# Kernel tuning notes

Hardware: AMD Instinct MI355X
Metric: run time of the kernel (lower is better)

Reference implementation:

```python
import jax, jax.numpy as jnp
import numpy as np

IN_DIM = 256
BOTTLENECK = 32
QK_DIM = IN_DIM // BOTTLENECK  # 8


def setup_inputs() -> dict:
    key = jax.random.key(0)
    ks = jax.random.split(key, 10)
    B, C, W, H = 4, IN_DIM, 64, 64
    s = 0.05
    return {
        "x": jax.random.normal(ks[0], (B, C, W, H), jnp.float32),
        "k": jax.random.normal(ks[1], (B, C, W, H), jnp.float32),
        "q": jax.random.normal(ks[2], (B, C, W, H), jnp.float32),
        "Wq": jax.random.normal(ks[3], (QK_DIM, C), jnp.float32) * s,
        "bq": jax.random.normal(ks[4], (QK_DIM,), jnp.float32) * s,
        "Wk": jax.random.normal(ks[5], (QK_DIM, C), jnp.float32) * s,
        "bk": jax.random.normal(ks[6], (QK_DIM,), jnp.float32) * s,
        "Wv": jax.random.normal(ks[7], (C, C), jnp.float32) * s,
        "bv": jax.random.normal(ks[8], (C,), jnp.float32) * s,
        "gamma": jnp.array([0.5], jnp.float32),
    }


def reference(x, k, q, Wq, bq, Wk, bk, Wv, bv, gamma):
    B, C, W, H = x.shape
    N = W * H
    # 1x1 convs == per-pixel linear maps over channels; flatten spatial to N
    xf = x.reshape(B, C, N)
    kf = k.reshape(B, C, N)
    qf = q.reshape(B, C, N)
    # proj_query: (B, N, d); proj_key: (B, d, N)
    pq = jnp.einsum('dc,bcn->bnd', Wq, qf) + bq[None, None, :]
    pk = jnp.einsum('dc,bcn->bdn', Wk, kf) + bk[None, :, None]
    energy = jnp.einsum('bnd,bdm->bnm', pq, pk)  # (B, N, N), un-scaled
    attention = jax.nn.softmax(energy, axis=-1)
    pv = jnp.einsum('ec,bcn->ben', Wv, xf) + bv[None, :, None]  # (B, C, N)
    # out = bmm(value, attention^T): out[b,c,n] = sum_m pv[b,c,m] * attn[b,n,m]
    out = jnp.einsum('bcm,bnm->bcn', pv, attention)
    out = out.reshape(B, C, W, H)
    out = gamma[0] * out + x
    return out, attention
```

## Files before the change

kernel.cpp:

```cpp
#include <hip/hip_runtime.h>

#define B_ 4
#define C_ 256
#define N_ 4096
#define D_ 8

typedef float f32x4 __attribute__((ext_vector_type(4)));
typedef __bf16 bf16x8 __attribute__((ext_vector_type(8)));

union U16 {
  bf16x8 v;
  unsigned short u[8];
  uint4 q;
};

__device__ inline unsigned short f2bf(float f) {
  unsigned int u = __float_as_uint(f);
  u = (u + 0x7FFFu + ((u >> 16) & 1u)) >> 16;
  return (unsigned short)u;
}

#define AS1 __attribute__((address_space(1)))
#define AS3 __attribute__((address_space(3)))
__device__ __forceinline__ void g2l16(const void* g, void* l) {
  __builtin_amdgcn_global_load_lds((AS1 const void*)g, (AS3 void*)l, 16, 0, 0);
}

__global__ void __launch_bounds__(256) k_pqk(
    const float* __restrict__ q, const float* __restrict__ k,
    const float* __restrict__ Wq, const float* __restrict__ bq,
    const float* __restrict__ Wk, const float* __restrict__ bk,
    float* __restrict__ pq_g, float* __restrict__ pk_g) {
  int b = blockIdx.y, n0 = blockIdx.x * 64;
  int t = threadIdx.x, nl = t & 63, sub = t >> 6;
  int n = n0 + nl;
  float aq[D_], ak[D_];
#pragma unroll
  for (int d = 0; d < D_; ++d) { aq[d] = 0.f; ak[d] = 0.f; }
  const float* qp = q + ((size_t)(b * C_ + sub * 64)) * N_ + n;
  const float* kp = k + ((size_t)(b * C_ + sub * 64)) * N_ + n;
  for (int cc = 0; cc < 64; ++cc) {
    int c = sub * 64 + cc;
    float qv = qp[(size_t)cc * N_];
    float kv = kp[(size_t)cc * N_];
#pragma unroll
    for (int d = 0; d < D_; ++d) {
      aq[d] = fmaf(Wq[d * C_ + c], qv, aq[d]);
      ak[d] = fmaf(Wk[d * C_ + c], kv, ak[d]);
    }
  }
  __shared__ float red[4][64][16];
#pragma unroll
  for (int d = 0; d < D_; ++d) { red[sub][nl][d] = aq[d]; red[sub][nl][8 + d] = ak[d]; }
  __syncthreads();
  if (t < 64) {
#pragma unroll
    for (int d = 0; d < D_; ++d) {
      float s = red[0][t][d] + red[1][t][d] + red[2][t][d] + red[3][t][d] + bq[d];
      pq_g[((size_t)b * N_ + n0 + t) * D_ + d] = s;
      float s2 = red[0][t][8 + d] + red[1][t][8 + d] + red[2][t][8 + d] + red[3][t][8 + d] + bk[d];
      pk_g[((size_t)b * D_ + d) * N_ + n0 + t] = s2;
    }
  }
}

__global__ void __launch_bounds__(256) k_pv(
    const float* __restrict__ x, const float* __restrict__ Wv,
    const float* __restrict__ bv, unsigned short* __restrict__ pv_g) {
  int b = blockIdx.y, n0 = blockIdx.x * 64;
  int t = threadIdx.x, lane = t & 63, w = t >> 6;
  __shared__ unsigned short xs[64][264];
  {
    int nl = t & 63, sub = t >> 6;
    for (int i = 0; i < 64; ++i) {
      int c = i * 4 + sub;
      float xv = x[((size_t)(b * C_ + c)) * N_ + n0 + nl];
      xs[nl][c] = f2bf(xv);
    }
  }
  __syncthreads();
  int e0 = w * 64;
  f32x4 acc[4][4];
#pragma unroll
  for (int mf = 0; mf < 4; ++mf)
#pragma unroll
    for (int nf = 0; nf < 4; ++nf) acc[mf][nf] = (f32x4)0.f;

  int rsel = lane & 15, koff = (lane >> 4) * 8;
  for (int kc = 0; kc < 8; ++kc) {
    int cbase = kc * 32 + koff;
    U16 afr[4];
#pragma unroll
    for (int mf = 0; mf < 4; ++mf) {
      const float* wp = Wv + (size_t)(e0 + mf * 16 + rsel) * C_ + cbase;
      float4 w0 = *(const float4*)wp;
      float4 w1 = *(const float4*)(wp + 4);
      afr[mf].u[0] = f2bf(w0.x); afr[mf].u[1] = f2bf(w0.y);
      afr[mf].u[2] = f2bf(w0.z); afr[mf].u[3] = f2bf(w0.w);
      afr[mf].u[4] = f2bf(w1.x); afr[mf].u[5] = f2bf(w1.y);
      afr[mf].u[6] = f2bf(w1.z); afr[mf].u[7] = f2bf(w1.w);
    }
    U16 bfr[4];
#pragma unroll
    for (int nf = 0; nf < 4; ++nf)
      bfr[nf].q = *(const uint4*)&xs[nf * 16 + rsel][cbase];
#pragma unroll
    for (int mf = 0; mf < 4; ++mf)
#pragma unroll
      for (int nf = 0; nf < 4; ++nf)
        acc[mf][nf] = __builtin_amdgcn_mfma_f32_16x16x32_bf16(afr[mf].v, bfr[nf].v, acc[mf][nf], 0, 0, 0);
  }
  int rowsub = (lane >> 4) * 4;
#pragma unroll
  for (int mf = 0; mf < 4; ++mf) {
#pragma unroll
    for (int nf = 0; nf < 4; ++nf) {
      int n = n0 + nf * 16 + rsel;
#pragma unroll
      for (int j = 0; j < 4; ++j) {
        int e = e0 + mf * 16 + rowsub + j;
        float v = acc[mf][nf][j] + bv[e];
        pv_g[((size_t)(b * C_ + e)) * N_ + n] = f2bf(v);
      }
    }
  }
}

__global__ void __launch_bounds__(256) k_rowsum(
    const float* __restrict__ pq_g, const float* __restrict__ pk_g,
    float* __restrict__ rinv_g) {
  int b = blockIdx.y, n0 = blockIdx.x * 32;
  int t = threadIdx.x, lane = t & 63, w = t >> 6;
  int r0 = n0 + w * 8;
  float pqr[8][D_];
#pragma unroll
  for (int r = 0; r < 8; ++r) {
    const float4* pp = (const float4*)(pq_g + ((size_t)b * N_ + r0 + r) * D_);
    float4 a = pp[0], c4 = pp[1];
    pqr[r][0] = a.x; pqr[r][1] = a.y; pqr[r][2] = a.z; pqr[r][3] = a.w;
    pqr[r][4] = c4.x; pqr[r][5] = c4.y; pqr[r][6] = c4.z; pqr[r][7] = c4.w;
  }
  float s[8];
#pragma unroll
  for (int r = 0; r < 8; ++r) s[r] = 0.f;
  const float* pkb = pk_g + (size_t)b * D_ * N_;
  for (int tt = 0; tt < 64; ++tt) {
    int m = tt * 64 + lane;
    float pkr[D_];
#pragma unroll
    for (int d = 0; d < D_; ++d) pkr[d] = pkb[(size_t)d * N_ + m];
#pragma unroll
    for (int r = 0; r < 8; ++r) {
      float e = pqr[r][0] * pkr[0];
#pragma unroll
      for (int d = 1; d < D_; ++d) e = fmaf(pqr[r][d], pkr[d], e);
      s[r] += __expf(e);
    }
  }
#pragma unroll
  for (int r = 0; r < 8; ++r) {
    float v = s[r];
    for (int off = 32; off; off >>= 1) v += __shfl_xor(v, off);
    s[r] = v;
  }
  if (lane == 0) {
#pragma unroll
    for (int r = 0; r < 8; ++r) rinv_g[(size_t)b * N_ + r0 + r] = 1.0f / s[r];
  }
}

__global__ void __launch_bounds__(512, 1) k_fused(
    const float* __restrict__ pq_g, const float* __restrict__ pk_g,
    const float* __restrict__ rinv_g, const unsigned short* __restrict__ pv_g,
    const float* __restrict__ x, const float* __restrict__ gamma,
    float* __restrict__ out_g, float* __restrict__ attn_g) {
  int bx = blockIdx.x;
  int b = bx & 3, grp = bx >> 2;
  int n0 = grp * 32;
  int t = threadIdx.x, lane = t & 63, w = t >> 6;
  int rsel = lane & 15, g = lane >> 4, koff = g * 8;
  int c0 = w * 32;
  int r0 = n0 + w * 4;

  __shared__ unsigned short pvs[2][256][64];
  __shared__ unsigned short asl[2][32][72];

  float pqr[4][D_], rinv[4];
#pragma unroll
  for (int rr = 0; rr < 4; ++rr) {
    const float4* pp = (const float4*)(pq_g + ((size_t)b * N_ + r0 + rr) * D_);
    float4 a = pp[0], c4 = pp[1];
    pqr[rr][0] = a.x; pqr[rr][1] = a.y; pqr[rr][2] = a.z; pqr[rr][3] = a.w;
    pqr[rr][4] = c4.x; pqr[rr][5] = c4.y; pqr[rr][6] = c4.z; pqr[rr][7] = c4.w;
    rinv[rr] = rinv_g[(size_t)b * N_ + r0 + rr];
  }

  const float* pkb = pk_g + (size_t)b * D_ * N_;
  const unsigned short* pvb = pv_g + (size_t)b * C_ * N_;
  float* attb = attn_g + ((size_t)b * N_ + r0) * N_;

  f32x4 acc[2][2];
#pragma unroll
  for (int mf = 0; mf < 2; ++mf)
#pragma unroll
    for (int cf = 0; cf < 2; ++cf) acc[mf][cf] = (f32x4)0.f;

#define STAGEPV(dstbuf, M0)                                                   \
  {                                                                           \
    _Pragma("unroll")                                                         \
    for (int i = 0; i < 4; ++i) {                                             \
      int c = c0 + i * 8 + (lane >> 3);                                       \
      int seg = lane & 7;                                                     \
      g2l16(pvb + (size_t)c * N_ + (M0) + ((seg ^ (c & 7)) << 3),             \
            &pvs[dstbuf][c0 + i * 8][0]);                                     \
    }                                                                         \
  }

  STAGEPV(0, 0)
  float pkr[D_];
#pragma unroll
  for (int d = 0; d < D_; ++d) pkr[d] = pkb[(size_t)d * N_ + lane];

  int cur = 0;
  for (int tt = 0; tt < 64; ++tt) {
    int m0 = tt * 64;
    bool more = (tt + 1 < 64);
    if (more) STAGEPV(cur ^ 1, m0 + 64)
    float pkn[D_];
    if (more) {
#pragma unroll
      for (int d = 0; d < D_; ++d) pkn[d] = pkb[(size_t)d * N_ + m0 + 64 + lane];
    }
#pragma unroll
    for (int rr = 0; rr < 4; ++rr) {
      float e = pqr[rr][0] * pkr[0];
#pragma unroll
      for (int d = 1; d < D_; ++d) e = fmaf(pqr[rr][d], pkr[d], e);
      float a = __expf(e) * rinv[rr];
      __builtin_nontemporal_store(a, attb + (size_t)rr * N_ + m0 + lane);
      asl[cur][w * 4 + rr][lane] = f2bf(a);
    }
    asm volatile("s_waitcnt lgkmcnt(0)" ::: "memory");
    __builtin_amdgcn_s_barrier();
    {
      U16 afr[2][2], bfr[2][2];
#pragma unroll
      for (int kf = 0; kf < 2; ++kf) {
#pragma unroll
        for (int mf = 0; mf < 2; ++mf)
          afr[kf][mf].q = *(const uint4*)&asl[cur][mf * 16 + rsel][kf * 32 + koff];
#pragma unroll
        for (int cf = 0; cf < 2; ++cf) {
          int c = c0 + cf * 16 + rsel;
          int sg = kf * 4 + g;
          bfr[kf][cf].q = *(const uint4*)&pvs[cur][c][(sg ^ (c & 7)) * 8];
        }
      }
#pragma unroll
      for (int kf = 0; kf < 2; ++kf)
#pragma unroll
        for (int mf = 0; mf < 2; ++mf)
#pragma unroll
          for (int cf = 0; cf < 2; ++cf)
            acc[mf][cf] = __builtin_amdgcn_mfma_f32_16x16x32_bf16(
                afr[kf][mf].v, bfr[kf][cf].v, acc[mf][cf], 0, 0, 0);
    }
#pragma unroll
    for (int d = 0; d < D_; ++d) pkr[d] = pkn[d];
    cur ^= 1;
  }
#undef STAGEPV
  float gm = gamma[0];
  int rowsub = g * 4;
#pragma unroll
  for (int mf = 0; mf < 2; ++mf) {
#pragma unroll
    for (int cf = 0; cf < 2; ++cf) {
      int c = c0 + cf * 16 + rsel;
      int nrow = n0 + mf * 16 + rowsub;
      const float4 xv = *(const float4*)(x + ((size_t)(b * C_ + c)) * N_ + nrow);
      float4 o;
      o.x = gm * acc[mf][cf][0] + xv.x;
      o.y = gm * acc[mf][cf][1] + xv.y;
      o.z = gm * acc[mf][cf][2] + xv.z;
      o.w = gm * acc[mf][cf][3] + xv.w;
      *(float4*)(out_g + ((size_t)(b * C_ + c)) * N_ + nrow) = o;
    }
  }
}

extern "C" void kernel_launch(void* const* d_in, const int* in_sizes, int n_in,
                              void* d_out, int out_size, void* d_ws, size_t ws_size,
                              hipStream_t stream) {
  const float* x  = (const float*)d_in[0];
  const float* k  = (const float*)d_in[1];
  const float* q  = (const float*)d_in[2];
  const float* Wq = (const float*)d_in[3];
  const float* bq = (const float*)d_in[4];
  const float* Wk = (const float*)d_in[5];
  const float* bk = (const float*)d_in[6];
  const float* Wv = (const float*)d_in[7];
  const float* bv = (const float*)d_in[8];
  const float* gamma = (const float*)d_in[9];

  float* out_g  = (float*)d_out;
  float* attn_g = out_g + (size_t)B_ * C_ * N_;

  char* ws = (char*)d_ws;
  float* pq_g = (float*)ws;
  float* pk_g = (float*)(ws + (1u << 19));
  float* rinv_g = (float*)(ws + (1u << 20));
  unsigned short* pv_g = (unsigned short*)(ws + (1u << 20) + (1u << 17));

  k_pqk<<<dim3(64, B_), 256, 0, stream>>>(q, k, Wq, bq, Wk, bk, pq_g, pk_g);
  k_pv<<<dim3(64, B_), 256, 0, stream>>>(x, Wv, bv, pv_g);
  k_rowsum<<<dim3(128, B_), 256, 0, stream>>>(pq_g, pk_g, rinv_g);
  k_fused<<<dim3(512), 512, 0, stream>>>(pq_g, pk_g, rinv_g, pv_g, x, gamma, out_g, attn_g);
}
```

Baseline: 161.1 us.

## Pre-swizzle PV into MFMA fragment layout and load directly from global

The PV projection kernel now writes its bf16 output in a fragment-ordered layout, so each lane's 16-byte MFMA B operand is one contiguous load. The fused attention kernel drops LDS staging of PV and reads B fragments straight from global/L2. It also shrinks blocks to 256 threads handling 16 rows, each wave covering 64 channels, with 1024 blocks and up to 4 blocks per CU. This removes LDS staging traffic and raises occupancy, but doubles the total PV reads from L2, since each block now covers half as many rows.

```diff
diff --git a/kernel.cpp b/kernel.cpp
--- a/kernel.cpp
+++ b/kernel.cpp
@@ -18,12 +18,6 @@
   unsigned int u = __float_as_uint(f);
   u = (u + 0x7FFFu + ((u >> 16) & 1u)) >> 16;
   return (unsigned short)u;
-}
-
-#define AS1 __attribute__((address_space(1)))
-#define AS3 __attribute__((address_space(3)))
-__device__ __forceinline__ void g2l16(const void* g, void* l) {
-  __builtin_amdgcn_global_load_lds((AS1 const void*)g, (AS3 void*)l, 16, 0, 0);
 }
 
 __global__ void __launch_bounds__(256) k_pqk(
@@ -66,7 +60,7 @@
 
 __global__ void __launch_bounds__(256) k_pv(
     const float* __restrict__ x, const float* __restrict__ Wv,
-    const float* __restrict__ bv, unsigned short* __restrict__ pv_g) {
+    const float* __restrict__ bv, unsigned short* __restrict__ pvF) {
   int b = blockIdx.y, n0 = blockIdx.x * 64;
   int t = threadIdx.x, lane = t & 63, w = t >> 6;
   __shared__ unsigned short xs[64][264];
@@ -110,17 +104,22 @@
       for (int nf = 0; nf < 4; ++nf)
         acc[mf][nf] = __builtin_amdgcn_mfma_f32_16x16x32_bf16(afr[mf].v, bfr[nf].v, acc[mf][nf], 0, 0, 0);
   }
+  unsigned short* pvFb = pvF + (size_t)b * C_ * N_;
   int rowsub = (lane >> 4) * 4;
 #pragma unroll
   for (int mf = 0; mf < 4; ++mf) {
 #pragma unroll
     for (int nf = 0; nf < 4; ++nf) {
       int n = n0 + nf * 16 + rsel;
+      int tt = n >> 6, m_in = n & 63;
+      int kf = m_in >> 5, rr2 = m_in & 31, g2 = rr2 >> 3, j2 = rr2 & 7;
 #pragma unroll
       for (int j = 0; j < 4; ++j) {
         int e = e0 + mf * 16 + rowsub + j;
         float v = acc[mf][nf][j] + bv[e];
-        pv_g[((size_t)(b * C_ + e)) * N_ + n] = f2bf(v);
+        int cg = e >> 4, cl = e & 15;
+        size_t word = ((size_t)(tt * 16 + cg) * 2 + kf) * 64 + g2 * 16 + cl;
+        pvFb[word * 8 + j2] = f2bf(v);
       }
     }
   }
@@ -169,21 +168,20 @@
   }
 }
 
-__global__ void __launch_bounds__(512, 1) k_fused(
+__global__ void __launch_bounds__(256, 4) k_fused(
     const float* __restrict__ pq_g, const float* __restrict__ pk_g,
-    const float* __restrict__ rinv_g, const unsigned short* __restrict__ pv_g,
+    const float* __restrict__ rinv_g, const unsigned short* __restrict__ pvF,
     const float* __restrict__ x, const float* __restrict__ gamma,
     float* __restrict__ out_g, float* __restrict__ attn_g) {
   int bx = blockIdx.x;
   int b = bx & 3, grp = bx >> 2;
-  int n0 = grp * 32;
+  int n0 = grp * 16;
   int t = threadIdx.x, lane = t & 63, w = t >> 6;
   int rsel = lane & 15, g = lane >> 4, koff = g * 8;
-  int c0 = w * 32;
+  int c0 = w * 64;
   int r0 = n0 + w * 4;
 
-  __shared__ unsigned short pvs[2][256][64];
-  __shared__ unsigned short asl[2][32][72];
+  __shared__ unsigned short asl[2][16][72];
 
   float pqr[4][D_], rinv[4];
 #pragma unroll
@@ -196,27 +194,13 @@
   }
 
   const float* pkb = pk_g + (size_t)b * D_ * N_;
-  const unsigned short* pvb = pv_g + (size_t)b * C_ * N_;
+  const unsigned short* pvFb = pvF + (size_t)b * C_ * N_;
   float* attb = attn_g + ((size_t)b * N_ + r0) * N_;
 
-  f32x4 acc[2][2];
-#pragma unroll
-  for (int mf = 0; mf < 2; ++mf)
-#pragma unroll
-    for (int cf = 0; cf < 2; ++cf) acc[mf][cf] = (f32x4)0.f;
-
-#define STAGEPV(dstbuf, M0)                                                   \
-  {                                                                           \
-    _Pragma("unroll")                                                         \
-    for (int i = 0; i < 4; ++i) {                                             \
-      int c = c0 + i * 8 + (lane >> 3);                                       \
-      int seg = lane & 7;                                                     \
-      g2l16(pvb + (size_t)c * N_ + (M0) + ((seg ^ (c & 7)) << 3),             \
-            &pvs[dstbuf][c0 + i * 8][0]);                                     \
-    }                                                                         \
-  }
-
-  STAGEPV(0, 0)
+  f32x4 acc[4];
+#pragma unroll
+  for (int cf = 0; cf < 4; ++cf) acc[cf] = (f32x4)0.f;
+
   float pkr[D_];
 #pragma unroll
   for (int d = 0; d < D_; ++d) pkr[d] = pkb[(size_t)d * N_ + lane];
@@ -225,7 +209,6 @@
   for (int tt = 0; tt < 64; ++tt) {
     int m0 = tt * 64;
     bool more = (tt + 1 < 64);
-    if (more) STAGEPV(cur ^ 1, m0 + 64)
     float pkn[D_];
     if (more) {
 #pragma unroll
@@ -243,49 +226,41 @@
     asm volatile("s_waitcnt lgkmcnt(0)" ::: "memory");
     __builtin_amdgcn_s_barrier();
     {
-      U16 afr[2][2], bfr[2][2];
+      U16 afr[2], bfr[2][4];
 #pragma unroll
       for (int kf = 0; kf < 2; ++kf) {
-#pragma unroll
-        for (int mf = 0; mf < 2; ++mf)
-          afr[kf][mf].q = *(const uint4*)&asl[cur][mf * 16 + rsel][kf * 32 + koff];
-#pragma unroll
-        for (int cf = 0; cf < 2; ++cf) {
-          int c = c0 + cf * 16 + rsel;
-          int sg = kf * 4 + g;
-          bfr[kf][cf].q = *(const uint4*)&pvs[cur][c][(sg ^ (c & 7)) * 8];
+        afr[kf].q = *(const uint4*)&asl[cur][rsel][kf * 32 + koff];
+#pragma unroll
+        for (int cf = 0; cf < 4; ++cf) {
+          int cg = (c0 >> 4) + cf;
+          bfr[kf][cf].q = *(const uint4*)(pvFb +
+              (((size_t)(tt * 16 + cg) * 2 + kf) * 64 + lane) * 8);
         }
       }
 #pragma unroll
       for (int kf = 0; kf < 2; ++kf)
 #pragma unroll
-        for (int mf = 0; mf < 2; ++mf)
-#pragma unroll
-          for (int cf = 0; cf < 2; ++cf)
-            acc[mf][cf] = __builtin_amdgcn_mfma_f32_16x16x32_bf16(
-                afr[kf][mf].v, bfr[kf][cf].v, acc[mf][cf], 0, 0, 0);
+        for (int cf = 0; cf < 4; ++cf)
+          acc[cf] = __builtin_amdgcn_mfma_f32_16x16x32_bf16(
+              afr[kf].v, bfr[kf][cf].v, acc[cf], 0, 0, 0);
     }
 #pragma unroll
     for (int d = 0; d < D_; ++d) pkr[d] = pkn[d];
     cur ^= 1;
   }
-#undef STAGEPV
   float gm = gamma[0];
   int rowsub = g * 4;
 #pragma unroll
-  for (int mf = 0; mf < 2; ++mf) {
-#pragma unroll
-    for (int cf = 0; cf < 2; ++cf) {
-      int c = c0 + cf * 16 + rsel;
-      int nrow = n0 + mf * 16 + rowsub;
-      const float4 xv = *(const float4*)(x + ((size_t)(b * C_ + c)) * N_ + nrow);
-      float4 o;
-      o.x = gm * acc[mf][cf][0] + xv.x;
-      o.y = gm * acc[mf][cf][1] + xv.y;
-      o.z = gm * acc[mf][cf][2] + xv.z;
-      o.w = gm * acc[mf][cf][3] + xv.w;
-      *(float4*)(out_g + ((size_t)(b * C_ + c)) * N_ + nrow) = o;
-    }
+  for (int cf = 0; cf < 4; ++cf) {
+    int c = c0 + cf * 16 + rsel;
+    int nrow = n0 + rowsub;
+    const float4 xv = *(const float4*)(x + ((size_t)(b * C_ + c)) * N_ + nrow);
+    float4 o;
+    o.x = gm * acc[cf][0] + xv.x;
+    o.y = gm * acc[cf][1] + xv.y;
+    o.z = gm * acc[cf][2] + xv.z;
+    o.w = gm * acc[cf][3] + xv.w;
+    *(float4*)(out_g + ((size_t)(b * C_ + c)) * N_ + nrow) = o;
   }
 }
 
@@ -310,10 +285,10 @@
   float* pq_g = (float*)ws;
   float* pk_g = (float*)(ws + (1u << 19));
   float* rinv_g = (float*)(ws + (1u << 20));
-  unsigned short* pv_g = (unsigned short*)(ws + (1u << 20) + (1u << 17));
+  unsigned short* pvF = (unsigned short*)(ws + (1u << 20) + (1u << 17));
 
   k_pqk<<<dim3(64, B_), 256, 0, stream>>>(q, k, Wq, bq, Wk, bk, pq_g, pk_g);
-  k_pv<<<dim3(64, B_), 256, 0, stream>>>(x, Wv, bv, pv_g);
+  k_pv<<<dim3(64, B_), 256, 0, stream>>>(x, Wv, bv, pvF);
   k_rowsum<<<dim3(128, B_), 256, 0, stream>>>(pq_g, pk_g, rinv_g);
-  k_fused<<<dim3(512), 512, 0, stream>>>(pq_g, pk_g, rinv_g, pv_g, x, gamma, out_g, attn_g);
-}
+  k_fused<<<dim3(1024), 256, 0, stream>>>(pq_g, pk_g, rinv_g, pvF, x, gamma, out_g, attn_g);
+}
```

New measurement: 199.7 us. +24.0%, slower.
